# Performance work log

Hardware: AMD Instinct MI355X
Metric: run time of the kernel (lower is better)

The kernel has to match this reference:

```python
import jax, jax.numpy as jnp
from jax import lax
import numpy as np

PATCH = 8
THRESHOLD = 0.2  # learned per-layer threshold, at init value


def conv2d(x, w, b, pad):
    # x: (N,C,H,W), w: (O,I,kh,kw)
    y = lax.conv_general_dilated(x, w, (1, 1), [(pad, pad), (pad, pad)],
                                 dimension_numbers=('NCHW', 'OIHW', 'NCHW'))
    return y + b[None, :, None, None]


def extract_patches(X, p):
    # Appends 4 positional channels, then splits into non-overlapping p x p patches.
    B, C, H, W = X.shape
    gy, gx = jnp.meshgrid(jnp.linspace(0.0, 1.0, H), jnp.linspace(0.0, 1.0, W), indexing='ij')
    pos = jnp.stack([gx, gy, jnp.sin(jnp.pi * gx), jnp.sin(jnp.pi * gy)]).astype(X.dtype)  # (4,H,W)
    Xc = jnp.concatenate([X, jnp.broadcast_to(pos[None], (B, 4, H, W))], axis=1)  # (B,C+4,H,W)
    h, w = H // p, W // p
    Xp = Xc.reshape(B, C + 4, h, p, w, p).transpose(0, 2, 4, 1, 3, 5).reshape(B, h * w, C + 4, p, p)
    return Xp, h, w


def _forward(X,
             proj_w0, proj_b0, exp_w0, exp_b0, fin_w0, fin_b0,
             proj_w1, proj_b1, exp_w1, exp_b1, fin_w1, fin_b1,
             proj_w2, proj_b2, exp_w2, exp_b2, fin_w2, fin_b2,
             proj_w3, proj_b3, exp_w3, exp_b3, fin_w3, fin_b3,
             router_w, router_b, lin_w, lin_b):
    layers = [
        (proj_w0, proj_b0, exp_w0, exp_b0, fin_w0, fin_b0),
        (proj_w1, proj_b1, exp_w1, exp_b1, fin_w1, fin_b1),
        (proj_w2, proj_b2, exp_w2, exp_b2, fin_w2, fin_b2),
        (proj_w3, proj_b3, exp_w3, exp_b3, fin_w3, fin_b3),
    ]
    for (pw, pb, ew, eb, fw, fb) in layers:
        Xp, h, w = extract_patches(X, PATCH)        # (B,P,C,p,p)
        B, P, C, pH, pW = Xp.shape
        flat = Xp.reshape(B * P, C, pH, pW)
        # router: conv-proj -> global avg pool -> linear -> softmax
        pooled = conv2d(flat, pw, pb, 1).mean(axis=(2, 3))                 # (BP, 8)
        scores = jax.nn.softmax(pooled @ router_w.T + router_b, axis=-1)  # (BP, E)
        scores = scores.reshape(B, P, -1)                                  # (B,P,E)
        # all experts as one grouped conv: (E,Co,C,3,3) -> (E*Co,C,3,3)
        E, Co = ew.shape[0], ew.shape[1]
        eo = conv2d(flat, ew.reshape(E * Co, C, 3, 3), eb.reshape(E * Co), 1)
        eo = jax.nn.relu(eo).reshape(B, P, E, Co, pH, pW)
        # expert is skipped unless some patch score exceeds the layer threshold
        gate = (scores.max(axis=(0, 1)) > THRESHOLD).astype(X.dtype)        # (E,)
        comb = jnp.einsum('bpechw,bpe->bpchw', eo, scores * gate[None, None, :])
        img = comb.reshape(B, h, w, Co, pH, pW).transpose(0, 3, 1, 4, 2, 5)
        img = img.reshape(B, Co, h * pH, w * pW)
        X = conv2d(img, fw, fb, 4)  # 1x1 conv, padding=4 -> H,W grow by 8
    return X.reshape(X.shape[0], -1) @ lin_w.T + lin_b


def setup_inputs() -> dict:
    key = jax.random.key(0)
    ks = iter(jax.random.split(key, 64))

    def nrm(shape, fan_in):
        return jax.random.normal(next(ks), shape, jnp.float32) / np.sqrt(fan_in)

    d = {"X": jax.random.normal(next(ks), (16, 3, 64, 64), jnp.float32)}
    cin = [7, 68, 68, 132]   # expert/key input channels per layer (prev out + 4 pos)
    cout = [64, 64, 128, 128]
    E = 4
    for l in range(4):
        d[f"proj_w{l}"] = nrm((8, cin[l], 3, 3), cin[l] * 9)
        d[f"proj_b{l}"] = jnp.zeros((8,), jnp.float32)
        d[f"exp_w{l}"] = nrm((E, cout[l], cin[l], 3, 3), cin[l] * 9)
        d[f"exp_b{l}"] = jnp.zeros((E, cout[l]), jnp.float32)
        d[f"fin_w{l}"] = nrm((cout[l], cout[l], 1, 1), cout[l])
        d[f"fin_b{l}"] = jnp.zeros((cout[l],), jnp.float32)
    d["router_w"] = nrm((E, 8), 8)
    d["router_b"] = jnp.zeros((E,), jnp.float32)
    feat = 128 * 96 * 96  # final (B,128,96,96) flattened
    d["lin_w"] = nrm((10, feat), feat)
    d["lin_b"] = jnp.zeros((10,), jnp.float32)
    return d


def reference(X,
              proj_w0, proj_b0, exp_w0, exp_b0, fin_w0, fin_b0,
              proj_w1, proj_b1, exp_w1, exp_b1, fin_w1, fin_b1,
              proj_w2, proj_b2, exp_w2, exp_b2, fin_w2, fin_b2,
              proj_w3, proj_b3, exp_w3, exp_b3, fin_w3, fin_b3,
              router_w, router_b, lin_w, lin_b):
    return _forward(X,
                    proj_w0, proj_b0, exp_w0, exp_b0, fin_w0, fin_b0,
                    proj_w1, proj_b1, exp_w1, exp_b1, fin_w1, fin_b1,
                    proj_w2, proj_b2, exp_w2, exp_b2, fin_w2, fin_b2,
                    proj_w3, proj_b3, exp_w3, exp_b3, fin_w3, fin_b3,
                    router_w, router_b, lin_w, lin_b)
```

## Files before the change

kernel.cpp:

```cpp
#include <hip/hip_runtime.h>
#include <math.h>

#define NB 16
#define NE 4
#define THRESH 0.2f
#define LIN_NS 64

typedef __attribute__((ext_vector_type(8))) _Float16 f16x8;
typedef __attribute__((ext_vector_type(4))) float f32x4;
typedef unsigned short u16;
typedef unsigned int u32;

__device__ inline u16 f16bits(float v) { _Float16 h = (_Float16)v; return __builtin_bit_cast(u16, h); }

__global__ void repack_all_kernel(const float* __restrict__ ew, const float* __restrict__ fw,
    u16* __restrict__ Wm, u16* __restrict__ Wp, u16* __restrict__ fW,
    int CO, int CIN, int CINp, int C) {
    const int M = NE * CO;
    const int n1 = 9 * M * CINp, n2 = M * 64, n3 = CO * CO;
    const int n = n1 + n2 + n3;
    for (int i = blockIdx.x * blockDim.x + threadIdx.x; i < n; i += gridDim.x * blockDim.x) {
        if (i < n1) {
            int k = i % CINp; int t = i / CINp; int m = t % M; int ij = t / M;
            float v = (k < CIN) ? ew[(m * C + k) * 9 + ij] : 0.f;
            Wm[i] = f16bits(v);
        } else if (i < n1 + n2) {
            int j = i - n1; int kp = j & 63; int m = j >> 6;
            float v = 0.f;
            if (CIN == 3) {
                if (kp < 27)      { int c = kp / 9,  ij = kp % 9;  v = ew[(m * C + c) * 9 + ij]; }
                else if (kp < 63) { int q = kp - 27; int pc = q / 9, ij = q % 9; v = ew[(m * C + 3 + pc) * 9 + ij]; }
            } else {
                if (kp < 36) { int pc = kp / 9, ij = kp % 9; v = ew[(m * C + CIN + pc) * 9 + ij]; }
            }
            Wp[j] = f16bits(v);
        } else {
            int j = i - n1 - n2;
            fW[j] = f16bits(fw[j]);
        }
    }
}

template<int CIN, int C>
__global__ __launch_bounds__(256) void router_kernel(
    const float* __restrict__ X, const float* __restrict__ pw, const float* __restrict__ pb,
    const float* __restrict__ rw, const float* __restrict__ rb,
    float* __restrict__ scores, int H, int W, int nP)
{
    __shared__ float S[4][C * 9 + 8];
    const int wv = threadIdx.x >> 6;
    const int lane = threadIdx.x & 63;
    const int bp = blockIdx.x * 4 + wv;
    const int P = nP * nP;
    const int b = bp / P, pi = bp % P;
    const int py = pi / nP, px = pi % nP;
    const int h = lane >> 3, w = lane & 7;
    const int gy = py * 8 + h, gx = px * 8 + w;
    float* Sw = S[wv];
    for (int c = 0; c < C; ++c) {
        float v;
        if (c < CIN) {
            v = X[(((size_t)b * CIN + c) * H + gy) * W + gx];
        } else {
            float t = (c == CIN || c == CIN + 2) ? gx * (1.f / (W - 1)) : gy * (1.f / (H - 1));
            v = (c >= CIN + 2) ? sinf(3.14159265358979323846f * t) : t;
        }
        float r = v;
        r += __shfl_xor(r, 1); r += __shfl_xor(r, 2); r += __shfl_xor(r, 4);
        float cc = v;
        cc += __shfl_xor(cc, 8); cc += __shfl_xor(cc, 16); cc += __shfl_xor(cc, 32);
        float T = r;
        T += __shfl_xor(T, 8); T += __shfl_xor(T, 16); T += __shfl_xor(T, 32);
        float R0 = __shfl(r, 0), R7 = __shfl(r, 56);
        float C0 = __shfl(cc, 0), C7 = __shfl(cc, 7);
        float x00 = __shfl(v, 0), x07 = __shfl(v, 7);
        float x70 = __shfl(v, 56), x77 = __shfl(v, 63);
        if (lane < 9) {
            int i = lane / 3, j = lane % 3;
            float s = T;
            if (i == 0) s -= R7; else if (i == 2) s -= R0;
            if (j == 0) s -= C7; else if (j == 2) s -= C0;
            if (i == 0 && j == 0) s += x77;
            else if (i == 0 && j == 2) s += x70;
            else if (i == 2 && j == 0) s += x07;
            else if (i == 2 && j == 2) s += x00;
            Sw[c * 9 + lane] = s;
        }
    }
    __syncthreads();
    if (lane < 8) {
        const int o = lane;
        float acc = 0.f;
        for (int c = 0; c < C; ++c) {
            #pragma unroll
            for (int ij = 0; ij < 9; ++ij)
                acc += pw[(o * C + c) * 9 + ij] * Sw[c * 9 + ij];
        }
        Sw[C * 9 + o] = acc * (1.f / 64.f) + pb[o];
    }
    __syncthreads();
    if (lane == 0) {
        float lg[NE];
        float m = -1e30f;
        #pragma unroll
        for (int e = 0; e < NE; ++e) {
            float a = rb[e];
            #pragma unroll
            for (int o = 0; o < 8; ++o) a += Sw[C * 9 + o] * rw[e * 8 + o];
            lg[e] = a;
            m = fmaxf(m, a);
        }
        float ssum = 0.f;
        #pragma unroll
        for (int e = 0; e < NE; ++e) { lg[e] = __expf(lg[e] - m); ssum += lg[e]; }
        float inv = 1.f / ssum;
        #pragma unroll
        for (int e = 0; e < NE; ++e) scores[bp * NE + e] = lg[e] * inv;
    }
}

__global__ __launch_bounds__(256) void border_kernel(float* __restrict__ Xn,
                                                     const float* __restrict__ fb,
                                                     int CO, int H, int W)
{
    const int Hout = H + 8, Wout = W + 8;
    const int nb = 16 * H + 64;
    const long total = (long)NB * CO * nb;
    for (long i = (long)blockIdx.x * blockDim.x + threadIdx.x; i < total;
         i += (long)gridDim.x * blockDim.x) {
        int j = (int)(i % nb); long t = i / nb; int o = (int)(t % CO); int b = (int)(t / CO);
        int y, x;
        if (j < 4 * Wout)       { y = j / Wout;             x = j % Wout; }
        else if (j < 8 * Wout)  { int j2 = j - 4 * Wout; y = H + 4 + j2 / Wout; x = j2 % Wout; }
        else                    { int j3 = j - 8 * Wout; y = 4 + j3 / 8;
                                  int c8 = j3 % 8; x = (c8 < 4) ? c8 : W + 4 + (c8 - 4); }
        Xn[(((size_t)b * CO + o) * Hout + y) * Wout + x] = fb[o];
    }
}

template<int CIN, int CINp, int CO>
__global__ __launch_bounds__(512, 2) void expert_fused_kernel(
    const float* __restrict__ X,
    const u16* __restrict__ Wm, const u16* __restrict__ Wp, const u16* __restrict__ fW,
    const float* __restrict__ eb, const float* __restrict__ fb,
    const float* __restrict__ scores, int BPtot,
    float* __restrict__ Xn, int H, int W, int nP)
{
    constexpr int M = NE * CO;
    constexpr int KSM = CINp / 32;
    constexpr int LOGK = (KSM == 4) ? 2 : (KSM == 2 ? 1 : 0);
    constexpr int NS = 9 * KSM;
    constexpr int SP = CINp + 8;
    constexpr int PIP = 72;
    constexpr int CP = CO + 8;
    constexpr bool FAT = (CO == 128);
    constexpr bool UNI = (CIN == 3);
    constexpr int NT = FAT ? 8 : 4;
    constexpr int PATW = 2 * 100 * SP;
    constexpr int POSW = 2 * 64 * PIP;
    constexpr int COMBW = 2 * 64 * CP;
    constexpr int SMW = (PATW + POSW > COMBW) ? (PATW + POSW) : COMBW;

    __shared__ __align__(16) u16 smem[SMW];
    __shared__ float pospix[2][4][64];
    __shared__ float xpix[2][3][64];
    __shared__ float gsh[8][NE];
    u16* pat = smem;
    u16* posim = smem + PATW;
    u16* comb = smem;

    const int P = nP * nP;
    const int bp0 = blockIdx.x * 2, bp1 = bp0 + 1;
    const int b0 = bp0 / P, pi0 = bp0 % P, py0 = pi0 / nP, px0 = pi0 % nP;
    const int b1 = bp1 / P, pi1 = bp1 % P, py1 = pi1 / nP, px1 = pi1 % nP;
    const int tid = threadIdx.x;
    const int Hout = H + 8, Wout = W + 8;

    if constexpr (!UNI) {
        for (int i = tid; i < 100 * SP; i += 512) ((u32*)pat)[i] = 0;
    }
    {
        int g = tid >> 8, r = tid & 255, pc = r >> 6, p = r & 63;
        int gy = (g ? py1 : py0) * 8 + (p >> 3), gx = (g ? px1 : px0) * 8 + (p & 7);
        float t = (pc == 0 || pc == 2) ? gx * (1.f / (W - 1)) : gy * (1.f / (H - 1));
        pospix[g][pc][p] = (pc >= 2) ? sinf(3.14159265358979323846f * t) : t;
    }
    if constexpr (UNI) {
        for (int i = tid; i < 2 * 3 * 64; i += 512) {
            int g = i / 192, r = i % 192, c = r >> 6, p = r & 63;
            int bb = g ? b1 : b0, py = g ? py1 : py0, px = g ? px1 : px0;
            xpix[g][c][p] = X[(((size_t)bb * CIN + c) * H + py * 8 + (p >> 3)) * W + px * 8 + (p & 7)];
        }
    }
    float gm[NE] = {-1e30f, -1e30f, -1e30f, -1e30f};
    for (int i = tid; i < BPtot; i += 512) {
        float4 sc = ((const float4*)scores)[i];
        gm[0] = fmaxf(gm[0], sc.x); gm[1] = fmaxf(gm[1], sc.y);
        gm[2] = fmaxf(gm[2], sc.z); gm[3] = fmaxf(gm[3], sc.w);
    }
    __syncthreads();

    if constexpr (!UNI) {
        for (int i = tid; i < 2 * CIN * 16; i += 512) {
            int g = i / (CIN * 16), j = i % (CIN * 16);
            int c = j >> 4, q = j & 15, h = q >> 1, w4 = (q & 1) * 4;
            int bb = g ? b1 : b0, py = g ? py1 : py0, px = g ? px1 : px0;
            const float4 v = *(const float4*)&X[(((size_t)bb * CIN + c) * H + py * 8 + h) * W + px * 8 + w4];
            int base = g * 100 * SP + c;
            pat[base + ((h + 1) * 10 + (w4 + 1)) * SP] = f16bits(v.x);
            pat[base + ((h + 1) * 10 + (w4 + 2)) * SP] = f16bits(v.y);
            pat[base + ((h + 1) * 10 + (w4 + 3)) * SP] = f16bits(v.z);
            pat[base + ((h + 1) * 10 + (w4 + 4)) * SP] = f16bits(v.w);
        }
    }
    for (int i = tid; i < 2 * 64 * 64; i += 512) {
        int g = i >> 12, r = i & 4095, pix = r >> 6, kp = r & 63;
        float v = 0.f;
        if constexpr (UNI) {
            if (kp < 27) {
                int c = kp / 9, ij = kp % 9;
                int hh = (pix >> 3) + ij / 3 - 1, ww = (pix & 7) + ij % 3 - 1;
                if (hh >= 0 && hh < 8 && ww >= 0 && ww < 8) v = xpix[g][c][hh * 8 + ww];
            } else if (kp < 63) {
                int q = kp - 27; int pc = q / 9, ij = q % 9;
                int hh = (pix >> 3) + ij / 3 - 1, ww = (pix & 7) + ij % 3 - 1;
                if (hh >= 0 && hh < 8 && ww >= 0 && ww < 8) v = pospix[g][pc][hh * 8 + ww];
            }
        } else {
            if (kp < 36) {
                int pc = kp / 9, ij = kp % 9;
                int hh = (pix >> 3) + ij / 3 - 1, ww = (pix & 7) + ij % 3 - 1;
                if (hh >= 0 && hh < 8 && ww >= 0 && ww < 8) v = pospix[g][pc][hh * 8 + ww];
            }
        }
        posim[g * 64 * PIP + pix * PIP + kp] = f16bits(v);
    }
    {
        const int lane = tid & 63, wvi = tid >> 6;
        #pragma unroll
        for (int e = 0; e < NE; ++e) {
            float v = gm[e];
            for (int o = 32; o; o >>= 1) v = fmaxf(v, __shfl_xor(v, o));
            gm[e] = v;
        }
        if (lane == 0) {
            #pragma unroll
            for (int e = 0; e < NE; ++e) gsh[wvi][e] = gm[e];
        }
    }
    __syncthreads();

    const int lane = tid & 63, wv = tid >> 6;
    const int colp = lane & 15, kg = lane >> 4;
    const int cot = FAT ? wv : (wv & 3);
    const int gO = FAT ? 0 : (wv >> 2);
    const int co0 = cot * 16;

    int prow[NT];
    #pragma unroll
    for (int nt = 0; nt < NT; ++nt) {
        int g = FAT ? (nt >> 2) : gO;
        int pix = (nt & 3) * 16 + colp;
        prow[nt] = g * 100 * SP + ((pix >> 3) * 10 + (pix & 7)) * SP;
    }
    int aoff[NE];
    #pragma unroll
    for (int e = 0; e < NE; ++e)
        aoff[e] = (e * CO + co0 + colp) * CINp + kg * 8;

    f32x4 acc[NE][NT];
    #pragma unroll
    for (int e = 0; e < NE; ++e)
        #pragma unroll
        for (int nt = 0; nt < NT; ++nt) acc[e][nt] = (f32x4){0.f, 0.f, 0.f, 0.f};

    f16x8 A0[NE], A1[NE];
    if constexpr (!UNI) {
        auto ldA = [&](int s, f16x8* A) {
            int ij = s >> LOGK, ks = s & (KSM - 1);
            const u16* Ws = Wm + (size_t)(ij * M) * CINp + ks * 32;
            #pragma unroll
            for (int e = 0; e < NE; ++e) A[e] = *(const f16x8*)(Ws + aoff[e]);
        };
        auto doStep = [&](int s, f16x8* A) {
            int ij = s >> LOGK, ks = s & (KSM - 1);
            int i3 = ij / 3;
            int tb = (i3 * 10 + (ij - 3 * i3)) * SP + ks * 32 + kg * 8;
            #pragma unroll
            for (int nt = 0; nt < NT; ++nt) {
                f16x8 Bv = *(const f16x8*)&pat[prow[nt] + tb];
                __builtin_amdgcn_s_setprio(1);
                #pragma unroll
                for (int e = 0; e < NE; ++e)
                    acc[e][nt] = __builtin_amdgcn_mfma_f32_16x16x32_f16(A[e], Bv, acc[e][nt], 0, 0, 0);
                __builtin_amdgcn_s_setprio(0);
            }
        };
        ldA(0, A0);
        int s = 0;
        for (; s + 1 < NS; s += 2) {
            ldA(s + 1, A1);
            doStep(s, A0);
            ldA((s + 2 < NS) ? s + 2 : s + 1, A0);
            doStep(s + 1, A1);
        }
        if (s < NS) doStep(s, A0);
    }

    #pragma unroll
    for (int ks = 0; ks < 2; ++ks) {
        #pragma unroll
        for (int e = 0; e < NE; ++e) {
            int ao = (e * CO + co0 + colp) * 64 + ks * 32 + kg * 8;
            A0[e] = *(const f16x8*)(Wp + ao);
        }
        #pragma unroll
        for (int nt = 0; nt < NT; ++nt) {
            int g = FAT ? (nt >> 2) : gO;
            int pix = (nt & 3) * 16 + colp;
            f16x8 Bv = *(const f16x8*)&posim[g * 64 * PIP + pix * PIP + ks * 32 + kg * 8];
            __builtin_amdgcn_s_setprio(1);
            #pragma unroll
            for (int e = 0; e < NE; ++e)
                acc[e][nt] = __builtin_amdgcn_mfma_f32_16x16x32_f16(A0[e], Bv, acc[e][nt], 0, 0, 0);
            __builtin_amdgcn_s_setprio(0);
        }
    }

    float sg0[NE], sg1[NE];
    #pragma unroll
    for (int e = 0; e < NE; ++e) {
        float mx = gsh[0][e];
        #pragma unroll
        for (int w8 = 1; w8 < 8; ++w8) mx = fmaxf(mx, gsh[w8][e]);
        float gv = (mx > THRESH) ? 1.f : 0.f;
        sg0[e] = scores[bp0 * NE + e] * gv;
        sg1[e] = scores[bp1 * NE + e] * gv;
    }
    float ebv[NE][4];
    #pragma unroll
    for (int e = 0; e < NE; ++e)
        #pragma unroll
        for (int r = 0; r < 4; ++r) ebv[e][r] = eb[e * CO + co0 + kg * 4 + r];

    __syncthreads();

    #pragma unroll
    for (int nt = 0; nt < NT; ++nt) {
        const int g = FAT ? (nt >> 2) : gO;
        int pix = (nt & 3) * 16 + colp;
        u16 hv[4];
        #pragma unroll
        for (int r = 0; r < 4; ++r) {
            float cv = 0.f;
            #pragma unroll
            for (int e = 0; e < NE; ++e) {
                float s2 = g ? sg1[e] : sg0[e];
                cv += s2 * fmaxf(acc[e][nt][r] + ebv[e][r], 0.f);
            }
            hv[r] = f16bits(cv);
        }
        uint2 q;
        q.x = (u32)hv[0] | ((u32)hv[1] << 16);
        q.y = (u32)hv[2] | ((u32)hv[3] << 16);
        *(uint2*)&comb[g * 64 * CP + pix * CP + co0 + kg * 4] = q;
    }
    __syncthreads();

    const int o0 = co0;
    f32x4 accF[NT];
    #pragma unroll
    for (int nt = 0; nt < NT; ++nt) accF[nt] = (f32x4){0.f, 0.f, 0.f, 0.f};
    #pragma unroll
    for (int ks = 0; ks < CO / 32; ++ks) {
        int ao = (o0 + colp) * CO + ks * 32 + kg * 8;
        f16x8 ah = *(const f16x8*)(fW + ao);
        __builtin_amdgcn_s_setprio(1);
        #pragma unroll
        for (int nt = 0; nt < NT; ++nt) {
            int g = FAT ? (nt >> 2) : gO;
            int pix = (nt & 3) * 16 + colp;
            f16x8 bv = *(const f16x8*)&comb[g * 64 * CP + pix * CP + ks * 32 + kg * 8];
            accF[nt] = __builtin_amdgcn_mfma_f32_16x16x32_f16(ah, bv, accF[nt], 0, 0, 0);
        }
        __builtin_amdgcn_s_setprio(0);
    }
    float fbv[4];
    #pragma unroll
    for (int r = 0; r < 4; ++r) fbv[r] = fb[o0 + kg * 4 + r];
    #pragma unroll
    for (int nt = 0; nt < NT; ++nt) {
        const int g = FAT ? (nt >> 2) : gO;
        int pix = (nt & 3) * 16 + colp;
        int bb = g ? b1 : b0, py = g ? py1 : py0, px = g ? px1 : px0;
        int gy = py * 8 + (pix >> 3) + 4, gx = px * 8 + (pix & 7) + 4;
        #pragma unroll
        for (int r = 0; r < 4; ++r) {
            int o = o0 + kg * 4 + r;
            Xn[(((size_t)bb * CO + o) * Hout + gy) * Wout + gx] = accF[nt][r] + fbv[r];
        }
    }
}

__global__ __launch_bounds__(256) void linear_part_kernel(
    const float* __restrict__ Xf, const float* __restrict__ lw, float* __restrict__ part)
{
    const int feat = 128 * 96 * 96;
    const int CH = feat / LIN_NS;
    const int s = blockIdx.x & (LIN_NS - 1);
    const int bg = blockIdx.x / LIN_NS;
    float acc[4][10];
    #pragma unroll
    for (int bb = 0; bb < 4; ++bb)
        #pragma unroll
        for (int o = 0; o < 10; ++o) acc[bb][o] = 0.f;
    const int n4 = CH / 4;
    for (int i = threadIdx.x; i < n4; i += 256) {
        float4 wv[10];
        #pragma unroll
        for (int o = 0; o < 10; ++o)
            wv[o] = *(const float4*)(lw + (size_t)o * feat + (size_t)s * CH + i * 4);
        #pragma unroll
        for (int bb = 0; bb < 4; ++bb) {
            float4 xv = *(const float4*)(Xf + (size_t)(bg * 4 + bb) * feat + (size_t)s * CH + i * 4);
            #pragma unroll
            for (int o = 0; o < 10; ++o)
                acc[bb][o] += xv.x * wv[o].x + xv.y * wv[o].y + xv.z * wv[o].z + xv.w * wv[o].w;
        }
    }
    #pragma unroll
    for (int bb = 0; bb < 4; ++bb)
        #pragma unroll
        for (int o = 0; o < 10; ++o)
            for (int m = 32; m; m >>= 1) acc[bb][o] += __shfl_xor(acc[bb][o], m);
    __shared__ float sm[4][40];
    int wvi = threadIdx.x >> 6, lane = threadIdx.x & 63;
    if (lane == 0) {
        #pragma unroll
        for (int bb = 0; bb < 4; ++bb)
            #pragma unroll
            for (int o = 0; o < 10; ++o) sm[wvi][bb * 10 + o] = acc[bb][o];
    }
    __syncthreads();
    int t = threadIdx.x;
    if (t < 40) {
        float a = sm[0][t] + sm[1][t] + sm[2][t] + sm[3][t];
        int bb = t / 10, o = t % 10;
        int b = bg * 4 + bb;
        part[(b * LIN_NS + s) * 10 + o] = a;
    }
}

__global__ __launch_bounds__(256) void linear_reduce_kernel(
    const float* __restrict__ part, const float* __restrict__ lb, float* __restrict__ out)
{
    int i = threadIdx.x;
    if (i < 160) {
        int b = i / 10, o = i % 10;
        float a = lb[o];
        for (int s = 0; s < LIN_NS; ++s) a += part[(b * LIN_NS + s) * 10 + o];
        out[i] = a;
    }
}

template<int CIN, int CINp, int CO>
static void run_layer(const float* Xin, int H, int nP, const float* const* Lw,
                      const float* rw, const float* rb,
                      const u16* Wm, const u16* Wp, const u16* fW,
                      float* scores, float* Xn, hipStream_t stream)
{
    const int W = H;
    const int BP = NB * nP * nP;
    const float* pw = Lw[0]; const float* pb = Lw[1];
    const float* ebias = Lw[3];
    const float* fb = Lw[5];

    router_kernel<CIN, CIN + 4><<<BP / 4, 256, 0, stream>>>(Xin, pw, pb, rw, rb, scores, H, W, nP);
    border_kernel<<<2048, 256, 0, stream>>>(Xn, fb, CO, H, W);
    expert_fused_kernel<CIN, CINp, CO><<<BP / 2, 512, 0, stream>>>(
        Xin, Wm, Wp, fW, ebias, fb, scores, BP, Xn, H, W, nP);
}

extern "C" void kernel_launch(void* const* d_in, const int* in_sizes, int n_in,
                              void* d_out, int out_size, void* d_ws, size_t ws_size,
                              hipStream_t stream)
{
    const float* X0 = (const float*)d_in[0];
    const float* L[4][6];
    for (int l = 0; l < 4; ++l)
        for (int k = 0; k < 6; ++k) L[l][k] = (const float*)d_in[1 + l * 6 + k];
    const float* rw = (const float*)d_in[25];
    const float* rb = (const float*)d_in[26];
    const float* lw = (const float*)d_in[27];
    const float* lb = (const float*)d_in[28];

    char* ws = (char*)d_ws;
    const size_t XA_B = 63438848;
    const size_t XB_B = 75497472;
    float* XA = (float*)(ws);
    float* XB = (float*)(ws + XA_B);
    char* wp = ws + XA_B + XB_B;
    const int cfg_CO[4]   = {64, 64, 128, 128};
    const int cfg_CINp[4] = {32, 64, 64, 128};
    u16 *Wm[4], *Wp[4], *fW[4];
    for (int l = 0; l < 4; ++l) {
        int M = NE * cfg_CO[l];
        Wm[l] = (u16*)wp;            wp += (size_t)9 * M * cfg_CINp[l] * 2;
        Wp[l] = (u16*)wp;            wp += (size_t)M * 64 * 2;
        fW[l] = (u16*)wp;            wp += (size_t)cfg_CO[l] * cfg_CO[l] * 2;
    }
    float* scores = (float*)wp;
    float* lpart = scores + 1936 * 4;

    const int cfg_CIN[4] = {3, 64, 64, 128};
    for (int l = 0; l < 4; ++l)
        repack_all_kernel<<<512, 256, 0, stream>>>(L[l][2], L[l][4], Wm[l], Wp[l], fW[l],
                                                   cfg_CO[l], cfg_CIN[l], cfg_CINp[l], cfg_CIN[l] + 4);

    run_layer<3,   32,  64>(X0, 64,  8, L[0], rw, rb, Wm[0], Wp[0], fW[0], scores, XA, stream);
    run_layer<64,  64,  64>(XA, 72,  9, L[1], rw, rb, Wm[1], Wp[1], fW[1], scores, XB, stream);
    run_layer<64,  64, 128>(XB, 80, 10, L[2], rw, rb, Wm[2], Wp[2], fW[2], scores, XA, stream);
    run_layer<128, 128, 128>(XA, 88, 11, L[3], rw, rb, Wm[3], Wp[3], fW[3], scores, XB, stream);

    linear_part_kernel<<<LIN_NS * (NB / 4), 256, 0, stream>>>(XB, lw, lpart);
    linear_reduce_kernel<<<1, 256, 0, stream>>>(lpart, lb, (float*)d_out);
}
```

Before: 787.7 us.

## Use 1024-thread blocks for CO=128 expert kernel, one patch per wave group

For the 128-output-channel layers, the fused expert kernel now launches 1024 threads. Each wave handles a single patch with four pixel tiles instead of both patches with eight. This halves the per-wave accumulator count (NE×NT), which cuts register pressure and allows more waves in flight. The FAT path also drops the double-buffered A-register prefetch in favour of a simple loop, which risks exposing more weight-load latency, and launch_bounds now ask for four blocks of 1024 threads.

```diff
diff --git a/kernel.cpp b/kernel.cpp
--- a/kernel.cpp
+++ b/kernel.cpp
@@ -139,7 +139,8 @@
 }
 
 template<int CIN, int CINp, int CO>
-__global__ __launch_bounds__(512, 2) void expert_fused_kernel(
+__global__ __launch_bounds__((CO == 128 ? 1024 : 512), (CO == 128 ? 4 : 2))
+void expert_fused_kernel(
     const float* __restrict__ X,
     const u16* __restrict__ Wm, const u16* __restrict__ Wp, const u16* __restrict__ fW,
     const float* __restrict__ eb, const float* __restrict__ fb,
@@ -155,7 +156,9 @@
     constexpr int CP = CO + 8;
     constexpr bool FAT = (CO == 128);
     constexpr bool UNI = (CIN == 3);
-    constexpr int NT = FAT ? 8 : 4;
+    constexpr int TPB = FAT ? 1024 : 512;
+    constexpr int WVS = TPB / 64;
+    constexpr int NT = 4;
     constexpr int PATW = 2 * 100 * SP;
     constexpr int POSW = 2 * 64 * PIP;
     constexpr int COMBW = 2 * 64 * CP;
@@ -164,7 +167,7 @@
     __shared__ __align__(16) u16 smem[SMW];
     __shared__ float pospix[2][4][64];
     __shared__ float xpix[2][3][64];
-    __shared__ float gsh[8][NE];
+    __shared__ float gsh[WVS][NE];
     u16* pat = smem;
     u16* posim = smem + PATW;
     u16* comb = smem;
@@ -177,23 +180,23 @@
     const int Hout = H + 8, Wout = W + 8;
 
     if constexpr (!UNI) {
-        for (int i = tid; i < 100 * SP; i += 512) ((u32*)pat)[i] = 0;
+        for (int i = tid; i < 100 * SP; i += TPB) ((u32*)pat)[i] = 0;
     }
     {
-        int g = tid >> 8, r = tid & 255, pc = r >> 6, p = r & 63;
+        int g = (tid >> 8) & 1, r = tid & 255, pc = r >> 6, p = r & 63;
         int gy = (g ? py1 : py0) * 8 + (p >> 3), gx = (g ? px1 : px0) * 8 + (p & 7);
         float t = (pc == 0 || pc == 2) ? gx * (1.f / (W - 1)) : gy * (1.f / (H - 1));
         pospix[g][pc][p] = (pc >= 2) ? sinf(3.14159265358979323846f * t) : t;
     }
     if constexpr (UNI) {
-        for (int i = tid; i < 2 * 3 * 64; i += 512) {
+        for (int i = tid; i < 2 * 3 * 64; i += TPB) {
             int g = i / 192, r = i % 192, c = r >> 6, p = r & 63;
             int bb = g ? b1 : b0, py = g ? py1 : py0, px = g ? px1 : px0;
             xpix[g][c][p] = X[(((size_t)bb * CIN + c) * H + py * 8 + (p >> 3)) * W + px * 8 + (p & 7)];
         }
     }
     float gm[NE] = {-1e30f, -1e30f, -1e30f, -1e30f};
-    for (int i = tid; i < BPtot; i += 512) {
+    for (int i = tid; i < BPtot; i += TPB) {
         float4 sc = ((const float4*)scores)[i];
         gm[0] = fmaxf(gm[0], sc.x); gm[1] = fmaxf(gm[1], sc.y);
         gm[2] = fmaxf(gm[2], sc.z); gm[3] = fmaxf(gm[3], sc.w);
@@ -201,7 +204,7 @@
     __syncthreads();
 
     if constexpr (!UNI) {
-        for (int i = tid; i < 2 * CIN * 16; i += 512) {
+        for (int i = tid; i < 2 * CIN * 16; i += TPB) {
             int g = i / (CIN * 16), j = i % (CIN * 16);
             int c = j >> 4, q = j & 15, h = q >> 1, w4 = (q & 1) * 4;
             int bb = g ? b1 : b0, py = g ? py1 : py0, px = g ? px1 : px0;
@@ -213,7 +216,7 @@
             pat[base + ((h + 1) * 10 + (w4 + 4)) * SP] = f16bits(v.w);
         }
     }
-    for (int i = tid; i < 2 * 64 * 64; i += 512) {
+    for (int i = tid; i < 2 * 64 * 64; i += TPB) {
         int g = i >> 12, r = i & 4095, pix = r >> 6, kp = r & 63;
         float v = 0.f;
         if constexpr (UNI) {
@@ -252,16 +255,15 @@
 
     const int lane = tid & 63, wv = tid >> 6;
     const int colp = lane & 15, kg = lane >> 4;
-    const int cot = FAT ? wv : (wv & 3);
-    const int gO = FAT ? 0 : (wv >> 2);
-    const int co0 = cot * 16;
+    const int co0 = FAT ? (wv & 7) * 16 : (wv & 3) * 16;
+    const int gW  = FAT ? (wv >> 3)     : (wv >> 2);
+    const int bpg = gW ? bp1 : bp0;
 
     int prow[NT];
     #pragma unroll
     for (int nt = 0; nt < NT; ++nt) {
-        int g = FAT ? (nt >> 2) : gO;
-        int pix = (nt & 3) * 16 + colp;
-        prow[nt] = g * 100 * SP + ((pix >> 3) * 10 + (pix & 7)) * SP;
+        int pix = nt * 16 + colp;
+        prow[nt] = gW * 100 * SP + ((pix >> 3) * 10 + (pix & 7)) * SP;
     }
     int aoff[NE];
     #pragma unroll
@@ -274,8 +276,27 @@
         #pragma unroll
         for (int nt = 0; nt < NT; ++nt) acc[e][nt] = (f32x4){0.f, 0.f, 0.f, 0.f};
 
-    f16x8 A0[NE], A1[NE];
-    if constexpr (!UNI) {
+    if constexpr (!UNI && FAT) {
+        for (int s = 0; s < NS; ++s) {
+            int ij = s >> LOGK, ks = s & (KSM - 1);
+            const u16* Ws = Wm + (size_t)(ij * M) * CINp + ks * 32;
+            f16x8 Ah[NE];
+            #pragma unroll
+            for (int e = 0; e < NE; ++e) Ah[e] = *(const f16x8*)(Ws + aoff[e]);
+            int i3 = ij / 3;
+            int tb = (i3 * 10 + (ij - 3 * i3)) * SP + ks * 32 + kg * 8;
+            #pragma unroll
+            for (int nt = 0; nt < NT; ++nt) {
+                f16x8 Bv = *(const f16x8*)&pat[prow[nt] + tb];
+                __builtin_amdgcn_s_setprio(1);
+                #pragma unroll
+                for (int e = 0; e < NE; ++e)
+                    acc[e][nt] = __builtin_amdgcn_mfma_f32_16x16x32_f16(Ah[e], Bv, acc[e][nt], 0, 0, 0);
+                __builtin_amdgcn_s_setprio(0);
+            }
+        }
+    } else if constexpr (!UNI) {
+        f16x8 A0[NE], A1[NE];
         auto ldA = [&](int s, f16x8* A) {
             int ij = s >> LOGK, ks = s & (KSM - 1);
             const u16* Ws = Wm + (size_t)(ij * M) * CINp + ks * 32;
@@ -309,33 +330,32 @@
 
     #pragma unroll
     for (int ks = 0; ks < 2; ++ks) {
+        f16x8 Ap[NE];
         #pragma unroll
         for (int e = 0; e < NE; ++e) {
             int ao = (e * CO + co0 + colp) * 64 + ks * 32 + kg * 8;
-            A0[e] = *(const f16x8*)(Wp + ao);
+            Ap[e] = *(const f16x8*)(Wp + ao);
         }
         #pragma unroll
         for (int nt = 0; nt < NT; ++nt) {
-            int g = FAT ? (nt >> 2) : gO;
-            int pix = (nt & 3) * 16 + colp;
-            f16x8 Bv = *(const f16x8*)&posim[g * 64 * PIP + pix * PIP + ks * 32 + kg * 8];
+            int pix = nt * 16 + colp;
+            f16x8 Bv = *(const f16x8*)&posim[gW * 64 * PIP + pix * PIP + ks * 32 + kg * 8];
             __builtin_amdgcn_s_setprio(1);
             #pragma unroll
             for (int e = 0; e < NE; ++e)
-                acc[e][nt] = __builtin_amdgcn_mfma_f32_16x16x32_f16(A0[e], Bv, acc[e][nt], 0, 0, 0);
+                acc[e][nt] = __builtin_amdgcn_mfma_f32_16x16x32_f16(Ap[e], Bv, acc[e][nt], 0, 0, 0);
             __builtin_amdgcn_s_setprio(0);
         }
     }
 
-    float sg0[NE], sg1[NE];
+    float sgW[NE];
     #pragma unroll
     for (int e = 0; e < NE; ++e) {
         float mx = gsh[0][e];
         #pragma unroll
-        for (int w8 = 1; w8 < 8; ++w8) mx = fmaxf(mx, gsh[w8][e]);
+        for (int w8 = 1; w8 < WVS; ++w8) mx = fmaxf(mx, gsh[w8][e]);
         float gv = (mx > THRESH) ? 1.f : 0.f;
-        sg0[e] = scores[bp0 * NE + e] * gv;
-        sg1[e] = scores[bp1 * NE + e] * gv;
+        sgW[e] = scores[bpg * NE + e] * gv;
     }
     float ebv[NE][4];
     #pragma unroll
@@ -347,23 +367,20 @@
 
     #pragma unroll
     for (int nt = 0; nt < NT; ++nt) {
-        const int g = FAT ? (nt >> 2) : gO;
-        int pix = (nt & 3) * 16 + colp;
+        int pix = nt * 16 + colp;
         u16 hv[4];
         #pragma unroll
         for (int r = 0; r < 4; ++r) {
             float cv = 0.f;
             #pragma unroll
-            for (int e = 0; e < NE; ++e) {
-                float s2 = g ? sg1[e] : sg0[e];
-                cv += s2 * fmaxf(acc[e][nt][r] + ebv[e][r], 0.f);
-            }
+            for (int e = 0; e < NE; ++e)
+                cv += sgW[e] * fmaxf(acc[e][nt][r] + ebv[e][r], 0.f);
             hv[r] = f16bits(cv);
         }
         uint2 q;
         q.x = (u32)hv[0] | ((u32)hv[1] << 16);
         q.y = (u32)hv[2] | ((u32)hv[3] << 16);
-        *(uint2*)&comb[g * 64 * CP + pix * CP + co0 + kg * 4] = q;
+        *(uint2*)&comb[gW * 64 * CP + pix * CP + co0 + kg * 4] = q;
     }
     __syncthreads();
 
@@ -378,9 +395,8 @@
         __builtin_amdgcn_s_setprio(1);
         #pragma unroll
         for (int nt = 0; nt < NT; ++nt) {
-            int g = FAT ? (nt >> 2) : gO;
-            int pix = (nt & 3) * 16 + colp;
-            f16x8 bv = *(const f16x8*)&comb[g * 64 * CP + pix * CP + ks * 32 + kg * 8];
+            int pix = nt * 16 + colp;
+            f16x8 bv = *(const f16x8*)&comb[gW * 64 * CP + pix * CP + ks * 32 + kg * 8];
             accF[nt] = __builtin_amdgcn_mfma_f32_16x16x32_f16(ah, bv, accF[nt], 0, 0, 0);
         }
         __builtin_amdgcn_s_setprio(0);
@@ -388,16 +404,15 @@
     float fbv[4];
     #pragma unroll
     for (int r = 0; r < 4; ++r) fbv[r] = fb[o0 + kg * 4 + r];
+    const int bbW = gW ? b1 : b0, pyW = gW ? py1 : py0, pxW = gW ? px1 : px0;
     #pragma unroll
     for (int nt = 0; nt < NT; ++nt) {
-        const int g = FAT ? (nt >> 2) : gO;
-        int pix = (nt & 3) * 16 + colp;
-        int bb = g ? b1 : b0, py = g ? py1 : py0, px = g ? px1 : px0;
-        int gy = py * 8 + (pix >> 3) + 4, gx = px * 8 + (pix & 7) + 4;
+        int pix = nt * 16 + colp;
+        int gy = pyW * 8 + (pix >> 3) + 4, gx = pxW * 8 + (pix & 7) + 4;
         #pragma unroll
         for (int r = 0; r < 4; ++r) {
             int o = o0 + kg * 4 + r;
-            Xn[(((size_t)bb * CO + o) * Hout + gy) * Wout + gx] = accF[nt][r] + fbv[r];
+            Xn[(((size_t)bbW * CO + o) * Hout + gy) * Wout + gx] = accF[nt][r] + fbv[r];
         }
     }
 }
@@ -474,10 +489,11 @@
     const float* pw = Lw[0]; const float* pb = Lw[1];
     const float* ebias = Lw[3];
     const float* fb = Lw[5];
+    constexpr int TPB = (CO == 128) ? 1024 : 512;
 
     router_kernel<CIN, CIN + 4><<<BP / 4, 256, 0, stream>>>(Xin, pw, pb, rw, rb, scores, H, W, nP);
     border_kernel<<<2048, 256, 0, stream>>>(Xn, fb, CO, H, W);
-    expert_fused_kernel<CIN, CINp, CO><<<BP / 2, 512, 0, stream>>>(
+    expert_fused_kernel<CIN, CINp, CO><<<BP / 2, TPB, 0, stream>>>(
         Xin, Wm, Wp, fW, ebias, fb, scores, BP, Xn, H, W, nP);
 }
 
```

New measurement: 968.7 us. 1.23x slower.
